# Optimization experiments

Hardware: AMD Instinct MI355X
Metric: run time of the kernel (lower is better)

The kernel has to match this reference:

```python
import jax, jax.numpy as jnp
import numpy as np

N_QUBITS = 12
N_LAYERS = 3
FEAT_DIM = 64
BATCH = 8192
PI = float(np.pi)


def setup_inputs() -> dict:
    key = jax.random.key(0)
    k1, k2, k3 = jax.random.split(key, 3)
    x = jax.random.normal(k1, (BATCH, FEAT_DIM), dtype=jnp.float32)
    # nn.Linear(feature_dim, num_qubits, bias=False) weight: [num_qubits, feature_dim]
    W = jax.random.normal(k2, (N_QUBITS, FEAT_DIM), dtype=jnp.float32) * (1.0 / np.sqrt(FEAT_DIM))
    # quantum params ~ Uniform(-pi, pi), shape [num_layers, num_qubits, 2] (RY, RZ angles)
    quantum_params = jax.random.uniform(k3, (N_LAYERS, N_QUBITS, 2), minval=-PI, maxval=PI, dtype=jnp.float32)
    return {"x": x, "W": W, "quantum_params": quantum_params}


def _halves(st, ax):
    a0 = jax.lax.index_in_dim(st, 0, ax, keepdims=True)
    a1 = jax.lax.index_in_dim(st, 1, ax, keepdims=True)
    return a0, a1


def _ry(st, theta, q, n):
    # RY(t) = [[cos t/2, -sin t/2], [sin t/2, cos t/2]] on qubit q (wire 0 = most significant)
    ax = q + 1
    c = jnp.cos(theta * 0.5)
    s = jnp.sin(theta * 0.5)
    if jnp.ndim(c) > 0:  # per-batch angles -> broadcast [B,1,...,1]
        c = c.reshape(c.shape + (1,) * n)
        s = s.reshape(s.shape + (1,) * n)
    a0, a1 = _halves(st, ax)
    return jnp.concatenate([c * a0 - s * a1, s * a0 + c * a1], axis=ax)


def _rz(st, theta, q, n):
    # RZ(t) = diag(e^{-i t/2}, e^{i t/2}) on qubit q
    ax = q + 1
    ph = jnp.exp(-0.5j * theta)
    a0, a1 = _halves(st, ax)
    return jnp.concatenate([ph * a0, jnp.conj(ph) * a1], axis=ax)


def _cnot(st, ctrl, tgt):
    # flip target amplitudes on the control=1 subspace
    ax_c, ax_t = ctrl + 1, tgt + 1
    s0, s1 = _halves(st, ax_c)
    return jnp.concatenate([s0, jnp.flip(s1, axis=ax_t)], axis=ax_c)


def reference(x, W, quantum_params):
    n = N_QUBITS
    # feature projection + tanh squashing to [-pi, pi]
    angles = jnp.tanh(x @ W.T) * PI  # [B, n]
    B = x.shape[0]
    # batched state vector |0...0>, shape [B] + [2]*n (wire 0 most significant, PennyLane convention)
    st = jnp.zeros((B,) + (2,) * n, dtype=jnp.complex64)
    st = st.at[(slice(None),) + (0,) * n].set(1.0)
    for layer in range(N_LAYERS):
        # data (re)uploading: RY(features[i]) each layer since data_reuploading=True
        for q in range(n):
            st = _ry(st, angles[:, q], q, n)
        # variational rotations
        for q in range(n):
            st = _ry(st, quantum_params[layer, q, 0], q, n)
            st = _rz(st, quantum_params[layer, q, 1], q, n)
        # ring entanglement
        for q in range(n):
            st = _cnot(st, q, (q + 1) % n)
    probs = jnp.real(st * jnp.conj(st))  # [B] + [2]*n
    outs = []
    for q in range(n):  # <PauliZ_q> = p(bit_q=0) - p(bit_q=1)
        axes = tuple(a for a in range(1, n + 1) if a != q + 1)
        p = probs.sum(axis=axes)  # [B, 2]
        outs.append(p[:, 0] - p[:, 1])
    return jnp.stack(outs, axis=1).astype(x.dtype)  # [B, n]
```

## Files before the change

kernel.cpp:

```cpp
#include <hip/hip_runtime.h>

namespace {

constexpr int NQ = 12;
constexpr int NL = 3;
constexpr int FEAT = 64;
constexpr float PI_F = 3.14159265358979323846f;

typedef float f2 __attribute__((ext_vector_type(2)));

constexpr int par12(unsigned x) { int p = 0; for (int i = 0; i < 12; ++i) p ^= (int)((x >> i) & 1u); return p; }
constexpr int lead12(unsigned x) { for (int k = 11; k >= 0; --k) if ((x >> k) & 1u) return k; return -1; }

struct Ech { unsigned v[16] = {}; int n = 0; };
constexpr unsigned ech_reduce(const Ech& E, unsigned x) {
  for (int i = 0; i < E.n; ++i) { int lb = lead12(E.v[i]); if (lb >= 0 && ((x >> lb) & 1u)) x ^= E.v[i]; }
  return x;
}
constexpr bool ech_add(Ech& E, unsigned x) {
  unsigned r = ech_reduce(E, x);
  if (!r) return false;
  int lb = lead12(r);
  int pos = E.n;
  for (int i = 0; i < E.n; ++i) { if (lead12(E.v[i]) < lb) { pos = i; break; } }
  for (int i = E.n; i > pos; --i) E.v[i] = E.v[i - 1];
  E.v[pos] = r; E.n++;
  return true;
}

constexpr unsigned apmat(const unsigned* rows, unsigned v) {
  unsigned o = 0; for (int k = 0; k < 12; ++k) if (par12(rows[k] & v)) o |= 1u << k; return o;
}
constexpr bool inv12(const unsigned* in, unsigned* out) {
  unsigned a[12] = {}, b[12] = {};
  for (int k = 0; k < 12; ++k) { a[k] = in[k]; b[k] = 1u << k; }
  for (int c = 0; c < 12; ++c) {
    int p = -1;
    for (int r = c; r < 12; ++r) if ((a[r] >> c) & 1u) { p = r; break; }
    if (p < 0) return false;
    unsigned t = a[c]; a[c] = a[p]; a[p] = t; t = b[c]; b[c] = b[p]; b[p] = t;
    for (int r = 0; r < 12; ++r) if (r != c && ((a[r] >> c) & 1u)) { a[r] ^= a[c]; b[r] ^= b[c]; }
  }
  for (int k = 0; k < 12; ++k) out[k] = b[k];
  return true;
}
constexpr unsigned dropb(unsigned x, int t) {
  unsigned lm = (1u << t) - 1u;
  return (x & lm) | ((x >> 1) & (0x7FFu & ~lm));
}

struct Logical {
  unsigned m[NL][NQ] = {}, rv[NL][NQ] = {}, rf[NQ] = {};
  bool ok = false;
};
constexpr Logical compute_raw() {
  Logical mp{};
  unsigned col[NQ] = {}, row[NQ] = {};
  for (int b = 0; b < NQ; ++b) { col[b] = 1u << b; row[b] = 1u << b; }
  mp.ok = true;
  for (int L = 0; L < NL; ++L) {
    for (int q = 0; q < NQ; ++q) {
      mp.m[L][q]  = col[NQ - 1 - q];
      mp.rv[L][q] = row[NQ - 1 - q];
      if (par12(mp.m[L][q] & mp.rv[L][q]) != 1) mp.ok = false;
    }
    for (int q = 0; q < NQ; ++q) {
      int bc = NQ - 1 - q;
      int bt = NQ - 1 - ((q + 1) % NQ);
      col[bc] ^= col[bt];
      row[bt] ^= row[bc];
    }
  }
  for (int q = 0; q < NQ; ++q) mp.rf[q] = row[NQ - 1 - q];
  return mp;
}

struct Plan {
  unsigned l0m[NQ] = {}, l0r[NQ] = {};
  unsigned gm[4][6] = {};
  unsigned gr[4][6] = {};
  unsigned rf[NQ] = {};
  unsigned phi[4][6] = {};
  unsigned coffE[4][64] = {};
  int cb[4] = {};
  bool ok = false;
};

constexpr bool findH(const Ech& G, unsigned rho, unsigned& out) {
  for (unsigned t = 0; t < 12; ++t) {
    unsigned v = 1u << t;
    if (par12(v & rho) == 0 && ech_reduce(G, v)) { out = v; return true; }
  }
  for (unsigned v = 1; v < 4096u; ++v) {
    if (par12(v & rho) == 0 && ech_reduce(G, v)) { out = v; return true; }
  }
  return false;
}

constexpr Plan build_plan() {
  Logical raw = compute_raw();
  Plan P{};
  P.ok = raw.ok;
  for (int q = 0; q < NQ; ++q) { P.l0m[q] = raw.m[0][q]; P.l0r[q] = raw.rv[0][q]; }
  unsigned fwd[12] = {}, invc[12] = {};
  for (int k = 0; k < 12; ++k) { fwd[k] = 1u << k; invc[k] = 1u << k; }
  for (int ph = 0; ph < 4; ++ph) {
    const int L = 1 + ph / 2, q0 = (ph % 2) * 6;
    unsigned ml[6] = {};
    for (int i = 0; i < 6; ++i) ml[i] = raw.m[L][q0 + i];
    bool done = false;
    for (int cbi = 5; cbi >= 0 && !done; --cbi) {
      unsigned rho = fwd[6 + cbi];
      bool bad = false;
      int idx = -1;
      for (int i = 0; i < 6; ++i) if (par12(ml[i] & rho)) { idx = i; break; }
      unsigned uc = 0;
      Ech W{};
      if (idx >= 0) {
        uc = ml[idx];
        for (int i = 0; i < 6; ++i) {
          if (i == idx) continue;
          unsigned w = par12(ml[i] & rho) ? (ml[i] ^ uc) : ml[i];
          ech_add(W, w);
        }
        if (W.n > 5) bad = true;
      } else {
        for (int i = 0; i < 6; ++i) ech_add(W, ml[i]);
        if (W.n > 5) bad = true;
        if (!bad) {
          bool got = false;
          for (unsigned t = 0; t < 12 && !got; ++t) {
            unsigned v = 1u << t;
            if (par12(v & rho)) { uc = v; got = true; }
          }
          if (!got) bad = true;
        }
      }
      if (bad) continue;
      Ech G{};
      for (int i = 0; i < W.n && !bad; ++i) if (!ech_add(G, W.v[i])) bad = true;
      if (!bad && !ech_add(G, uc)) bad = true;
      if (bad) continue;
      unsigned regH[5] = {};
      int nH = W.n;
      for (int i = 0; i < nH; ++i) regH[i] = W.v[i];
      for (int slot = nH; slot < 5 && !bad; ++slot) {
        unsigned v = 0;
        if (!findH(G, rho, v)) { bad = true; break; }
        regH[slot] = v; ech_add(G, v);
      }
      if (bad) continue;
      unsigned lam[6] = {};
      for (int j = 0; j < 6 && !bad; ++j) {
        unsigned cand = invc[j];
        if (par12(cand & rho) != 0 || !ech_reduce(G, cand)) {
          if (!findH(G, rho, cand)) { bad = true; break; }
        }
        lam[j] = cand; ech_add(G, cand);
      }
      if (bad) continue;
      unsigned ncols[12] = {};
      for (int j = 0; j < 6; ++j) ncols[j] = lam[j];
      {
        int w = 0;
        for (int k = 0; k < 6; ++k) ncols[6 + k] = (k == cbi) ? uc : regH[w++];
      }
      unsigned Mrows[12] = {};
      for (int k = 0; k < 12; ++k) {
        unsigned r = 0;
        for (int j = 0; j < 12; ++j) r |= ((ncols[j] >> k) & 1u) << j;
        Mrows[k] = r;
      }
      unsigned fnew[12] = {};
      if (!inv12(Mrows, fnew)) continue;
      bool okp = true;
      unsigned gmv[6] = {}, grv[6] = {};
      for (int i = 0; i < 6 && okp; ++i) {
        unsigned SM = apmat(fnew, ml[i]);
        if (SM & 63u) okp = false;
        unsigned sg = 0;
        for (int k = 0; k < 12; ++k) if (par12(raw.rv[L][q0 + i] & ncols[k])) sg |= 1u << k;
        if (par12(SM & sg) != 1) okp = false;
        gmv[i] = SM; grv[i] = sg;
      }
      unsigned phj[6] = {}, Ust[6] = {};
      for (int j = 0; j < 6 && okp; ++j) {
        phj[j] = apmat(fwd, lam[j]);
        if ((phj[j] >> (6 + cbi)) & 1u) okp = false;
      }
      for (int k = 0; k < 6 && okp; ++k) {
        Ust[k] = apmat(fwd, ncols[6 + k]);
        if (((Ust[k] >> (6 + cbi)) & 1u) != (unsigned)(k == cbi ? 1 : 0)) okp = false;
      }
      if (!okp) continue;
      P.cb[ph] = cbi;
      for (int j = 0; j < 6; ++j) P.phi[ph][j] = phj[j];
      for (int rp = 0; rp < 64; ++rp) {
        unsigned psi = 0;
        for (int i = 0; i < 6; ++i) if ((rp >> i) & 1) psi ^= Ust[i];
        P.coffE[ph][rp] = dropb(psi, 6 + cbi);
      }
      for (int i = 0; i < 6; ++i) { P.gm[ph][i] = gmv[i]; P.gr[ph][i] = grv[i]; }
      for (int k = 0; k < 12; ++k) { fwd[k] = fnew[k]; invc[k] = ncols[k]; }
      done = true;
    }
    if (!done) { P.ok = false; return P; }
  }
  for (int q = 0; q < NQ; ++q) {
    unsigned sg = 0;
    for (int k = 0; k < 12; ++k) if (par12(raw.rf[q] & invc[k])) sg |= 1u << k;
    P.rf[q] = sg;
  }
  return P;
}

constexpr Plan PLAN = build_plan();
static_assert(PLAN.ok, "plan construction failed");

__device__ __forceinline__ f2 pk_mul_bl(f2 a, f2 u) {
  f2 d;
  asm("v_pk_mul_f32 %0, %1, %2 op_sel:[0,0] op_sel_hi:[1,0]" : "=v"(d) : "v"(a), "v"(u));
  return d;
}
__device__ __forceinline__ f2 pk_fma_rot_p(f2 a, f2 u, f2 c) {
  f2 d;
  asm("v_pk_fma_f32 %0, %1, %2, %3 op_sel:[1,1,0] op_sel_hi:[0,1,1] neg_lo:[1,0,0]"
      : "=v"(d) : "v"(a), "v"(u), "v"(c));
  return d;
}
__device__ __forceinline__ f2 pk_fma_rot_m(f2 a, f2 u, f2 c) {
  f2 d;
  asm("v_pk_fma_f32 %0, %1, %2, %3 op_sel:[1,1,0] op_sel_hi:[0,1,1] neg_hi:[1,0,0]"
      : "=v"(d) : "v"(a), "v"(u), "v"(c));
  return d;
}
__device__ __forceinline__ f2 pk_fma_bl_p(f2 p, f2 v, f2 c) {
  f2 d;
  asm("v_pk_fma_f32 %0, %1, %2, %3 op_sel:[0,0,0] op_sel_hi:[1,0,1]"
      : "=v"(d) : "v"(p), "v"(v), "v"(c));
  return d;
}
__device__ __forceinline__ f2 pk_fma_bl_m(f2 p, f2 v, f2 c) {
  f2 d;
  asm("v_pk_fma_f32 %0, %1, %2, %3 op_sel:[0,0,0] op_sel_hi:[1,0,1] neg_lo:[0,1,0] neg_hi:[0,1,0]"
      : "=v"(d) : "v"(p), "v"(v), "v"(c));
  return d;
}
__device__ __forceinline__ f2 pk_mul_d(f2 a, f2 b) {
  f2 d;
  asm("v_pk_mul_f32 %0, %1, %2" : "=v"(d) : "v"(a), "v"(b));
  return d;
}
__device__ __forceinline__ f2 pk_fma_d(f2 a, f2 b, f2 c) {
  f2 d;
  asm("v_pk_fma_f32 %0, %1, %2, %3" : "=v"(d) : "v"(a), "v"(b), "v"(c));
  return d;
}

template<bool REAL>
__device__ __forceinline__ f2 updp(f2 a, f2 p, f2 u, f2 v) {
  if constexpr (REAL) return pk_fma_bl_p(p, v, pk_mul_bl(a, u));
  else return pk_fma_rot_p(p, v, pk_fma_bl_p(p, v, pk_fma_rot_p(a, u, pk_mul_bl(a, u))));
}
template<bool REAL>
__device__ __forceinline__ f2 updm(f2 a, f2 p, f2 u, f2 v) {
  if constexpr (REAL) return pk_fma_bl_m(p, v, pk_mul_bl(a, u));
  else return pk_fma_rot_p(p, v, pk_fma_bl_m(p, v, pk_fma_rot_m(a, u, pk_mul_bl(a, u))));
}

template<unsigned MLO>
__device__ __forceinline__ float shx(float v, int lane4) {
  if constexpr (MLO == 0u) {
    return v;
  } else if constexpr (MLO < 32u) {
    constexpr int off = (int)((MLO << 10) | 0x1fu);
    return __int_as_float(__builtin_amdgcn_ds_swizzle(__float_as_int(v), off));
  } else {
    int addr = lane4 ^ (int)(MLO << 2);
    return __int_as_float(__builtin_amdgcn_ds_bpermute(addr, __float_as_int(v)));
  }
}

template<unsigned M, unsigned R, int NREG, bool REAL>
__device__ __forceinline__ void gate(f2* st, float ghalf, float phihalf, int lane, int lane4) {
  float s, c;
  __sincosf(ghalf, &s, &c);
  constexpr unsigned MHI = (M >> 6) & 63u;
  constexpr unsigned MLO = M & 63u;
  constexpr unsigned RHI = (R >> 6) & 63u;
  constexpr unsigned RLO = R & 63u;
  float sL = (__popc((int)(RLO & (unsigned)lane)) & 1) ? -1.f : 1.f;
  f2 u, v;
  if constexpr (REAL) {
    u.x = c;       u.y = 0.f;
    v.x = -s * sL; v.y = 0.f;
  } else {
    float sf, cf;
    __sincosf(phihalf, &sf, &cf);
    u.x = c * cf;         u.y = (-c * sf) * sL;
    v.x = (-s * cf) * sL; v.y = s * sf;
  }
  if constexpr (MLO == 0u) {
    constexpr unsigned TB = MHI & (~MHI + 1u);
    #pragma unroll
    for (int r = 0; r < NREG; ++r) {
      if ((r & (int)TB) == 0) {
        int r2 = r ^ (int)MHI;
        const bool rp = ((__builtin_popcount((unsigned)r & RHI)) & 1) != 0;
        f2 a = st[r], b = st[r2];
        st[r]  = rp ? updm<REAL>(a, b, u, v) : updp<REAL>(a, b, u, v);
        st[r2] = rp ? updp<REAL>(b, a, u, v) : updm<REAL>(b, a, u, v);
      }
    }
  } else {
    #pragma unroll
    for (int r = 0; r < NREG; ++r) {
      f2 p;
      p.x = shx<MLO>(st[r].x, lane4);
      p.y = shx<MLO>(st[r].y, lane4);
      const bool rp = ((__builtin_popcount((unsigned)r & RHI)) & 1) != 0;
      st[r] = rp ? updm<REAL>(st[r], p, u, v) : updp<REAL>(st[r], p, u, v);
    }
  }
}

template<int Q>
__device__ __forceinline__ void l0_lane(f2* st, const float* ang, const float* __restrict__ qp, int lane, int lane4) {
  if constexpr (Q < NQ) {
    constexpr unsigned M = PLAN.l0m[Q];
    if constexpr (M < 64u) {
      gate<M, PLAN.l0r[Q], 1, false>(st, 0.5f * (ang[Q] + qp[Q * 2 + 0]), 0.5f * qp[Q * 2 + 1], lane, lane4);
    }
    l0_lane<Q + 1>(st, ang, qp, lane, lane4);
  }
}
template<int Q, unsigned DONE>
__device__ __forceinline__ void l0_reg(f2* st, const float* ang, const float* __restrict__ qp) {
  if constexpr (Q < NQ) {
    constexpr unsigned M = PLAN.l0m[Q];
    if constexpr (M >= 64u) {
      constexpr unsigned TB = (M >> 6) & 63u;
      float sh = 0.5f * (ang[Q] + qp[Q * 2 + 0]);
      float ph = 0.5f * qp[Q * 2 + 1];
      float s, c, sf, cf;
      __sincosf(sh, &s, &c);
      __sincosf(ph, &sf, &cf);
      f2 u0; u0.x = c * cf; u0.y = -c * sf;
      f2 u1; u1.x = s * cf; u1.y =  s * sf;
      #pragma unroll
      for (int r = 0; r < 64; ++r) {
        if ((r & ~(int)DONE & 63) == 0) {
          f2 a = st[r];
          int r2 = r | (int)TB;
          st[r]  = pk_fma_rot_p(a, u0, pk_mul_bl(a, u0));
          st[r2] = pk_fma_rot_p(a, u1, pk_mul_bl(a, u1));
        }
      }
      l0_reg<Q + 1, DONE | TB>(st, ang, qp);
    } else {
      l0_reg<Q + 1, DONE>(st, ang, qp);
    }
  }
}

__device__ __forceinline__ int pad(int a) { return a + (a >> 5); }

template<int PH>
__device__ __forceinline__ void remap(f2* st, f2* lds, int lane) {
  constexpr int b = PLAN.cb[PH];
  constexpr unsigned LM6 = (1u << b) - 1u;
  constexpr unsigned LM = (1u << (6 + b)) - 1u;
  unsigned B = 0;
  #pragma unroll
  for (int j = 0; j < 6; ++j) B ^= (unsigned)(-(int)((lane >> j) & 1)) & PLAN.phi[PH][j];
  unsigned rBe = (B & LM) | ((B >> 1) & (0x7FFu & ~LM));
  #pragma unroll
  for (int s = 0; s < 2; ++s) {
    #pragma unroll
    for (int r = 0; r < 64; ++r) {
      if (((r >> b) & 1) == s) {
        const int cr = (r & (int)LM6) | ((r >> 1) & (31 & ~(int)LM6));
        lds[pad((cr << 6) | lane)] = st[r];
      }
    }
    asm volatile("s_waitcnt lgkmcnt(0)" ::: "memory");
    #pragma unroll
    for (int rp = 0; rp < 64; ++rp) {
      if (((rp >> b) & 1) == s) {
        st[rp] = lds[pad((int)(rBe ^ PLAN.coffE[PH][rp]))];
      }
    }
    asm volatile("s_waitcnt lgkmcnt(0)" ::: "memory");
  }
}

template<int PH, int I>
__device__ __forceinline__ void do_phase(f2* st, const float* ang, const float* __restrict__ qp, int lane, int lane4) {
  if constexpr (I < 6) {
    constexpr int L = 1 + PH / 2;
    constexpr bool REAL = (L == NL - 1);
    constexpr int q = (PH % 2) * 6 + I;
    constexpr unsigned M = PLAN.gm[PH][I];
    constexpr unsigned R = PLAN.gr[PH][I];
    float th0 = qp[(L * NQ + q) * 2 + 0];
    float ph1 = REAL ? 0.f : 0.5f * qp[(L * NQ + q) * 2 + 1];
    gate<M, R, 64, REAL>(st, 0.5f * (ang[q] + th0), ph1, lane, lane4);
    do_phase<PH, I + 1>(st, ang, qp, lane, lane4);
  }
}

__device__ __forceinline__ float redsum(float v, int lane4) {
  v += shx<1>(v, lane4);
  v += shx<2>(v, lane4);
  v += shx<4>(v, lane4);
  v += shx<8>(v, lane4);
  v += shx<16>(v, lane4);
  v += shx<32>(v, lane4);
  return v;
}
__device__ __forceinline__ float fast_tanh(float x) {
  float e = __expf(2.f * x);
  float r = __builtin_amdgcn_rcpf(e + 1.f);
  return 1.f - 2.f * r;
}

template<int Q>
__device__ __forceinline__ void finish(const f2* acc6, float& outv, int lane, int lane4) {
  if constexpr (Q < NQ) {
    constexpr unsigned RLO = PLAN.rf[Q] & 63u;
    float a = (Q & 1) ? acc6[Q / 2].y : acc6[Q / 2].x;
    float sLn = (__popc((int)(RLO & (unsigned)lane)) & 1) ? -a : a;
    float t = redsum(sLn, lane4);
    if (lane == Q) outv = t;
    finish<Q + 1>(acc6, outv, lane, lane4);
  }
}

__global__ __launch_bounds__(64, 1) void qtr_kernel(const float* __restrict__ x,
                                                    const float* __restrict__ W,
                                                    const float* __restrict__ qp,
                                                    float* __restrict__ out) {
  __shared__ f2 ldsb[2112];
  int b = blockIdx.x;
  int lane = threadIdx.x;
  int lane4 = lane << 2;

  float xv = x[b * FEAT + lane];
  float ang[NQ];
  #pragma unroll
  for (int q = 0; q < NQ; ++q) {
    float prod = redsum(xv * W[q * FEAT + lane], lane4);
    ang[q] = PI_F * fast_tanh(prod);
  }

  f2 st[64];
  st[0].x = (lane == 0) ? 1.f : 0.f;
  st[0].y = 0.f;

  l0_lane<0>(st, ang, qp, lane, lane4);
  l0_reg<0, 0u>(st, ang, qp);

  remap<0>(st, ldsb, lane);
  do_phase<0, 0>(st, ang, qp, lane, lane4);
  remap<1>(st, ldsb, lane);
  do_phase<1, 0>(st, ang, qp, lane, lane4);
  remap<2>(st, ldsb, lane);
  do_phase<2, 0>(st, ang, qp, lane, lane4);
  remap<3>(st, ldsb, lane);
  do_phase<3, 0>(st, ang, qp, lane, lane4);

  f2 acc6[6];
  #pragma unroll
  for (int j = 0; j < 6; ++j) { acc6[j].x = 0.f; acc6[j].y = 0.f; }
  #pragma unroll
  for (int r = 0; r < 64; ++r) {
    f2 q2 = pk_mul_d(st[r], st[r]);
    float p = q2.x + q2.y;
    f2 pp; pp.x = p; pp.y = p;
    #pragma unroll
    for (int j = 0; j < 6; ++j) {
      const bool n0 = ((__builtin_popcount(((PLAN.rf[2 * j]     >> 6) & 63u) & (unsigned)r)) & 1) != 0;
      const bool n1 = ((__builtin_popcount(((PLAN.rf[2 * j + 1] >> 6) & 63u) & (unsigned)r)) & 1) != 0;
      f2 sg; sg.x = n0 ? -1.f : 1.f; sg.y = n1 ? -1.f : 1.f;
      acc6[j] = pk_fma_d(pp, sg, acc6[j]);
    }
  }

  float outv = 0.f;
  finish<0>(acc6, outv, lane, lane4);

  if (lane < NQ) out[b * NQ + lane] = outv;
}

}

extern "C" void kernel_launch(void* const* d_in, const int* in_sizes, int n_in,
                              void* d_out, int out_size, void* d_ws, size_t ws_size,
                              hipStream_t stream) {
  const float* x  = (const float*)d_in[0];
  const float* W  = (const float*)d_in[1];
  const float* qp = (const float*)d_in[2];
  float* out = (float*)d_out;
  qtr_kernel<<<8192, 64, 0, stream>>>(x, W, qp, out);
}
```

Before: 131.9 us.

## Split each sample's state vector across two waves with LDS exchange

Each block now uses two 64-lane waves, and each wave holds half of the 4096-amplitude state (32 registers instead of 64). Gates on the top register bit become cross-wave exchanges through LDS with __syncthreads, and remaps and the final reduction are rewritten for the split layout. The aim is to halve register pressure per wave and double parallelism per sample. The cost is extra block-level barriers, LDS traffic for cross-wave gates, and duplicated angle computation in both waves.

```diff
diff --git a/kernel.cpp b/kernel.cpp
--- a/kernel.cpp
+++ b/kernel.cpp
@@ -217,6 +217,10 @@
 constexpr Plan PLAN = build_plan();
 static_assert(PLAN.ok, "plan construction failed");
 
+constexpr int find_qw() { for (int q = 0; q < NQ; ++q) if (((PLAN.l0m[q] >> 6) & 63u) == 32u) return q; return -1; }
+constexpr int QW = find_qw();
+static_assert(QW >= 0, "no wave-bit l0 gate found");
+
 __device__ __forceinline__ f2 pk_mul_bl(f2 a, f2 u) {
   f2 d;
   asm("v_pk_mul_f32 %0, %1, %2 op_sel:[0,0] op_sel_hi:[1,0]" : "=v"(d) : "v"(a), "v"(u));
@@ -267,6 +271,7 @@
   if constexpr (REAL) return pk_fma_bl_m(p, v, pk_mul_bl(a, u));
   else return pk_fma_rot_p(p, v, pk_fma_bl_m(p, v, pk_fma_rot_m(a, u, pk_mul_bl(a, u))));
 }
+__device__ __forceinline__ f2 cmul(f2 a, f2 u) { return pk_fma_rot_p(a, u, pk_mul_bl(a, u)); }
 
 template<unsigned MLO>
 __device__ __forceinline__ float shx(float v, int lane4) {
@@ -281,16 +286,34 @@
   }
 }
 
-template<unsigned M, unsigned R, int NREG, bool REAL>
-__device__ __forceinline__ void gate(f2* st, float ghalf, float phihalf, int lane, int lane4) {
+template<unsigned M, unsigned R, bool REAL>
+__device__ __forceinline__ void gate1(f2* st, float ghalf, float phihalf, int lane, int lane4) {
   float s, c;
   __sincosf(ghalf, &s, &c);
-  constexpr unsigned MHI = (M >> 6) & 63u;
   constexpr unsigned MLO = M & 63u;
-  constexpr unsigned RHI = (R >> 6) & 63u;
   constexpr unsigned RLO = R & 63u;
   float sL = (__popc((int)(RLO & (unsigned)lane)) & 1) ? -1.f : 1.f;
   f2 u, v;
+  float sf, cf;
+  __sincosf(phihalf, &sf, &cf);
+  u.x = c * cf;         u.y = (-c * sf) * sL;
+  v.x = (-s * cf) * sL; v.y = s * sf;
+  f2 p;
+  p.x = shx<MLO>(st[0].x, lane4);
+  p.y = shx<MLO>(st[0].y, lane4);
+  st[0] = updp<REAL>(st[0], p, u, v);
+}
+
+template<unsigned R, bool REAL>
+__device__ __forceinline__ void make_uv(float ghalf, float phihalf, int l6, int w, f2& u, f2& v) {
+  constexpr unsigned RHI = (R >> 6) & 63u;
+  constexpr unsigned RLO = R & 63u;
+  constexpr unsigned S5 = (RHI >> 5) & 1u;
+  float s, c;
+  __sincosf(ghalf, &s, &c);
+  int par = __popc((int)(RLO & (unsigned)l6));
+  if constexpr (S5 != 0u) par ^= w;
+  float sL = (par & 1) ? -1.f : 1.f;
   if constexpr (REAL) {
     u.x = c;       u.y = 0.f;
     v.x = -s * sL; v.y = 0.f;
@@ -300,27 +323,72 @@
     u.x = c * cf;         u.y = (-c * sf) * sL;
     v.x = (-s * cf) * sL; v.y = s * sf;
   }
-  if constexpr (MLO == 0u) {
-    constexpr unsigned TB = MHI & (~MHI + 1u);
-    #pragma unroll
-    for (int r = 0; r < NREG; ++r) {
-      if ((r & (int)TB) == 0) {
-        int r2 = r ^ (int)MHI;
-        const bool rp = ((__builtin_popcount((unsigned)r & RHI)) & 1) != 0;
-        f2 a = st[r], b = st[r2];
-        st[r]  = rp ? updm<REAL>(a, b, u, v) : updp<REAL>(a, b, u, v);
-        st[r2] = rp ? updp<REAL>(b, a, u, v) : updm<REAL>(b, a, u, v);
-      }
-    }
-  } else {
-    #pragma unroll
-    for (int r = 0; r < NREG; ++r) {
-      f2 p;
-      p.x = shx<MLO>(st[r].x, lane4);
-      p.y = shx<MLO>(st[r].y, lane4);
-      const bool rp = ((__builtin_popcount((unsigned)r & RHI)) & 1) != 0;
-      st[r] = rp ? updm<REAL>(st[r], p, u, v) : updp<REAL>(st[r], p, u, v);
-    }
+}
+
+template<unsigned M, unsigned R, bool REAL>
+__device__ __forceinline__ void gate32_local(f2* st, float ghalf, float phihalf, int l6, int w) {
+  constexpr unsigned MHI = (M >> 6) & 31u;
+  constexpr unsigned RHI5 = (R >> 6) & 31u;
+  static_assert(MHI != 0u, "empty local mask");
+  f2 u, v;
+  make_uv<R, REAL>(ghalf, phihalf, l6, w, u, v);
+  constexpr unsigned TB = MHI & (~MHI + 1u);
+  #pragma unroll
+  for (int rl = 0; rl < 32; ++rl) {
+    if ((rl & (int)TB) == 0) {
+      int rl2 = rl ^ (int)MHI;
+      const bool rp = ((__builtin_popcount((unsigned)rl & RHI5)) & 1) != 0;
+      f2 a = st[rl], b = st[rl2];
+      st[rl]  = rp ? updm<REAL>(a, b, u, v) : updp<REAL>(a, b, u, v);
+      st[rl2] = rp ? updp<REAL>(b, a, u, v) : updm<REAL>(b, a, u, v);
+    }
+  }
+}
+
+template<unsigned M, unsigned R, bool REAL>
+__device__ __forceinline__ void gate32_cross(f2* st, f2* lds, float ghalf, float phihalf, int l6, int w) {
+  constexpr unsigned MHI = (M >> 6) & 63u;
+  constexpr unsigned ML5 = MHI & 31u;
+  constexpr unsigned RHI5 = (R >> 6) & 31u;
+  constexpr int FLIP = (int)((ML5 >> 4) & 1u);
+  f2 u, v;
+  make_uv<R, REAL>(ghalf, phihalf, l6, w, u, v);
+  #pragma unroll
+  for (int t = 0; t < 2; ++t) {
+    if (w == 0) {
+      #pragma unroll
+      for (int rr = 0; rr < 16; ++rr) {
+        const int rlm = (t << 4) | rr;
+        lds[(rr << 6) | l6] = st[rlm];
+      }
+    } else {
+      #pragma unroll
+      for (int rr = 0; rr < 16; ++rr) {
+        const int rlm = ((t ^ FLIP) << 4) | rr;
+        const int i = (rlm ^ (int)ML5) & 15;
+        lds[1024 | (i << 6) | l6] = st[rlm];
+      }
+    }
+    __syncthreads();
+    if (w == 0) {
+      #pragma unroll
+      for (int rr = 0; rr < 16; ++rr) {
+        const int rlm = (t << 4) | rr;
+        f2 p = lds[1024 | (rr << 6) | l6];
+        const bool rp = ((__builtin_popcount((unsigned)rlm & RHI5)) & 1) != 0;
+        st[rlm] = rp ? updm<REAL>(st[rlm], p, u, v) : updp<REAL>(st[rlm], p, u, v);
+      }
+    } else {
+      #pragma unroll
+      for (int rr = 0; rr < 16; ++rr) {
+        const int rlm = ((t ^ FLIP) << 4) | rr;
+        const int i = (rlm ^ (int)ML5) & 15;
+        f2 p = lds[(i << 6) | l6];
+        const bool rp = ((__builtin_popcount((unsigned)rlm & RHI5)) & 1) != 0;
+        st[rlm] = rp ? updm<REAL>(st[rlm], p, u, v) : updp<REAL>(st[rlm], p, u, v);
+      }
+    }
+    __syncthreads();
   }
 }
 
@@ -329,17 +397,17 @@
   if constexpr (Q < NQ) {
     constexpr unsigned M = PLAN.l0m[Q];
     if constexpr (M < 64u) {
-      gate<M, PLAN.l0r[Q], 1, false>(st, 0.5f * (ang[Q] + qp[Q * 2 + 0]), 0.5f * qp[Q * 2 + 1], lane, lane4);
+      gate1<M, PLAN.l0r[Q], false>(st, 0.5f * (ang[Q] + qp[Q * 2 + 0]), 0.5f * qp[Q * 2 + 1], lane, lane4);
     }
     l0_lane<Q + 1>(st, ang, qp, lane, lane4);
   }
 }
 template<int Q, unsigned DONE>
-__device__ __forceinline__ void l0_reg(f2* st, const float* ang, const float* __restrict__ qp) {
+__device__ __forceinline__ void l0_reg32(f2* st, const float* ang, const float* __restrict__ qp) {
   if constexpr (Q < NQ) {
     constexpr unsigned M = PLAN.l0m[Q];
-    if constexpr (M >= 64u) {
-      constexpr unsigned TB = (M >> 6) & 63u;
+    if constexpr (M >= 64u && ((M >> 6) & 63u) != 32u) {
+      constexpr unsigned TB = (M >> 6) & 31u;
       float sh = 0.5f * (ang[Q] + qp[Q * 2 + 0]);
       float ph = 0.5f * qp[Q * 2 + 1];
       float s, c, sf, cf;
@@ -348,17 +416,17 @@
       f2 u0; u0.x = c * cf; u0.y = -c * sf;
       f2 u1; u1.x = s * cf; u1.y =  s * sf;
       #pragma unroll
-      for (int r = 0; r < 64; ++r) {
-        if ((r & ~(int)DONE & 63) == 0) {
+      for (int r = 0; r < 32; ++r) {
+        if ((r & ~(int)DONE & 31) == 0) {
           f2 a = st[r];
           int r2 = r | (int)TB;
-          st[r]  = pk_fma_rot_p(a, u0, pk_mul_bl(a, u0));
-          st[r2] = pk_fma_rot_p(a, u1, pk_mul_bl(a, u1));
-        }
-      }
-      l0_reg<Q + 1, DONE | TB>(st, ang, qp);
+          st[r]  = cmul(a, u0);
+          st[r2] = cmul(a, u1);
+        }
+      }
+      l0_reg32<Q + 1, DONE | TB>(st, ang, qp);
     } else {
-      l0_reg<Q + 1, DONE>(st, ang, qp);
+      l0_reg32<Q + 1, DONE>(st, ang, qp);
     }
   }
 }
@@ -366,46 +434,82 @@
 __device__ __forceinline__ int pad(int a) { return a + (a >> 5); }
 
 template<int PH>
-__device__ __forceinline__ void remap(f2* st, f2* lds, int lane) {
+__device__ __forceinline__ void remap32(f2* st, f2* lds, int l6, int w) {
   constexpr int b = PLAN.cb[PH];
-  constexpr unsigned LM6 = (1u << b) - 1u;
   constexpr unsigned LM = (1u << (6 + b)) - 1u;
   unsigned B = 0;
   #pragma unroll
-  for (int j = 0; j < 6; ++j) B ^= (unsigned)(-(int)((lane >> j) & 1)) & PLAN.phi[PH][j];
+  for (int j = 0; j < 6; ++j) B ^= (unsigned)(-(int)((l6 >> j) & 1)) & PLAN.phi[PH][j];
   unsigned rBe = (B & LM) | ((B >> 1) & (0x7FFu & ~LM));
-  #pragma unroll
-  for (int s = 0; s < 2; ++s) {
+  if constexpr (b == 5) {
     #pragma unroll
-    for (int r = 0; r < 64; ++r) {
-      if (((r >> b) & 1) == s) {
-        const int cr = (r & (int)LM6) | ((r >> 1) & (31 & ~(int)LM6));
-        lds[pad((cr << 6) | lane)] = st[r];
-      }
-    }
-    asm volatile("s_waitcnt lgkmcnt(0)" ::: "memory");
+    for (int s = 0; s < 2; ++s) {
+      if (w == s) {
+        #pragma unroll
+        for (int rl = 0; rl < 32; ++rl) lds[pad((rl << 6) | l6)] = st[rl];
+      }
+      __syncthreads();
+      if (w == s) {
+        #pragma unroll
+        for (int rl = 0; rl < 32; ++rl) st[rl] = lds[pad((int)(rBe ^ PLAN.coffE[PH][rl | (s << 5)]))];
+      }
+      __syncthreads();
+    }
+  } else {
+    constexpr unsigned LM5 = (1u << b) - 1u;
     #pragma unroll
-    for (int rp = 0; rp < 64; ++rp) {
-      if (((rp >> b) & 1) == s) {
-        st[rp] = lds[pad((int)(rBe ^ PLAN.coffE[PH][rp]))];
-      }
-    }
-    asm volatile("s_waitcnt lgkmcnt(0)" ::: "memory");
+    for (int s = 0; s < 2; ++s) {
+      if (w == 0) {
+        #pragma unroll
+        for (int rl = 0; rl < 32; ++rl) {
+          if (((rl >> b) & 1) == s) {
+            const int cr = (rl & (int)LM5) | ((rl >> 1) & (15 & ~(int)LM5));
+            lds[pad((cr << 6) | l6)] = st[rl];
+          }
+        }
+      } else {
+        #pragma unroll
+        for (int rl = 0; rl < 32; ++rl) {
+          if (((rl >> b) & 1) == s) {
+            const int cr = 16 | (rl & (int)LM5) | ((rl >> 1) & (15 & ~(int)LM5));
+            lds[pad((cr << 6) | l6)] = st[rl];
+          }
+        }
+      }
+      __syncthreads();
+      if (w == 0) {
+        #pragma unroll
+        for (int rl = 0; rl < 32; ++rl) {
+          if (((rl >> b) & 1) == s) st[rl] = lds[pad((int)(rBe ^ PLAN.coffE[PH][rl]))];
+        }
+      } else {
+        #pragma unroll
+        for (int rl = 0; rl < 32; ++rl) {
+          if (((rl >> b) & 1) == s) st[rl] = lds[pad((int)(rBe ^ PLAN.coffE[PH][rl | 32]))];
+        }
+      }
+      __syncthreads();
+    }
   }
 }
 
 template<int PH, int I>
-__device__ __forceinline__ void do_phase(f2* st, const float* ang, const float* __restrict__ qp, int lane, int lane4) {
+__device__ __forceinline__ void do_phase(f2* st, f2* lds, const float* ang, const float* __restrict__ qp, int l6, int w) {
   if constexpr (I < 6) {
     constexpr int L = 1 + PH / 2;
     constexpr bool REAL = (L == NL - 1);
     constexpr int q = (PH % 2) * 6 + I;
     constexpr unsigned M = PLAN.gm[PH][I];
     constexpr unsigned R = PLAN.gr[PH][I];
+    static_assert((M & 63u) == 0u, "phase gate not reg-local");
     float th0 = qp[(L * NQ + q) * 2 + 0];
     float ph1 = REAL ? 0.f : 0.5f * qp[(L * NQ + q) * 2 + 1];
-    gate<M, R, 64, REAL>(st, 0.5f * (ang[q] + th0), ph1, lane, lane4);
-    do_phase<PH, I + 1>(st, ang, qp, lane, lane4);
+    float g = 0.5f * (ang[q] + th0);
+    if constexpr (((M >> 11) & 1u) != 0u)
+      gate32_cross<M, R, REAL>(st, lds, g, ph1, l6, w);
+    else
+      gate32_local<M, R, REAL>(st, g, ph1, l6, w);
+    do_phase<PH, I + 1>(st, lds, ang, qp, l6, w);
   }
 }
 
@@ -425,71 +529,102 @@
 }
 
 template<int Q>
-__device__ __forceinline__ void finish(const f2* acc6, float& outv, int lane, int lane4) {
+__device__ __forceinline__ void finish(const f2* acc6, float& outv, int l6, int lane4, int w) {
   if constexpr (Q < NQ) {
     constexpr unsigned RLO = PLAN.rf[Q] & 63u;
+    constexpr unsigned S11 = (PLAN.rf[Q] >> 11) & 1u;
     float a = (Q & 1) ? acc6[Q / 2].y : acc6[Q / 2].x;
-    float sLn = (__popc((int)(RLO & (unsigned)lane)) & 1) ? -a : a;
+    int par = __popc((int)(RLO & (unsigned)l6));
+    if constexpr (S11 != 0u) par ^= w;
+    float sLn = (par & 1) ? -a : a;
     float t = redsum(sLn, lane4);
-    if (lane == Q) outv = t;
-    finish<Q + 1>(acc6, outv, lane, lane4);
-  }
-}
-
-__global__ __launch_bounds__(64, 1) void qtr_kernel(const float* __restrict__ x,
-                                                    const float* __restrict__ W,
-                                                    const float* __restrict__ qp,
-                                                    float* __restrict__ out) {
+    if (l6 == Q) outv = t;
+    finish<Q + 1>(acc6, outv, l6, lane4, w);
+  }
+}
+
+__global__ __launch_bounds__(128) void qtr_kernel(const float* __restrict__ x,
+                                                  const float* __restrict__ W,
+                                                  const float* __restrict__ qp,
+                                                  float* __restrict__ out) {
   __shared__ f2 ldsb[2112];
-  int b = blockIdx.x;
-  int lane = threadIdx.x;
-  int lane4 = lane << 2;
-
-  float xv = x[b * FEAT + lane];
+  int bb = blockIdx.x;
+  int tid = threadIdx.x;
+  int w = tid >> 6;
+  int l6 = tid & 63;
+  int lane4 = l6 << 2;
+
+  float xv = x[bb * FEAT + l6];
   float ang[NQ];
   #pragma unroll
   for (int q = 0; q < NQ; ++q) {
-    float prod = redsum(xv * W[q * FEAT + lane], lane4);
+    float prod = redsum(xv * W[q * FEAT + l6], lane4);
     ang[q] = PI_F * fast_tanh(prod);
   }
 
-  f2 st[64];
-  st[0].x = (lane == 0) ? 1.f : 0.f;
-  st[0].y = 0.f;
-
-  l0_lane<0>(st, ang, qp, lane, lane4);
-  l0_reg<0, 0u>(st, ang, qp);
-
-  remap<0>(st, ldsb, lane);
-  do_phase<0, 0>(st, ang, qp, lane, lane4);
-  remap<1>(st, ldsb, lane);
-  do_phase<1, 0>(st, ang, qp, lane, lane4);
-  remap<2>(st, ldsb, lane);
-  do_phase<2, 0>(st, ang, qp, lane, lane4);
-  remap<3>(st, ldsb, lane);
-  do_phase<3, 0>(st, ang, qp, lane, lane4);
+  f2 st[32];
+  if (w == 0) {
+    st[0].x = (l6 == 0) ? 1.f : 0.f;
+    st[0].y = 0.f;
+    l0_lane<0>(st, ang, qp, l6, lane4);
+    l0_reg32<0, 0u>(st, ang, qp);
+  }
+  {
+    float sh = 0.5f * (ang[QW] + qp[QW * 2 + 0]);
+    float ph = 0.5f * qp[QW * 2 + 1];
+    float s, c, sf, cf;
+    __sincosf(sh, &s, &c);
+    __sincosf(ph, &sf, &cf);
+    f2 u0; u0.x = c * cf; u0.y = -c * sf;
+    f2 u1; u1.x = s * cf; u1.y =  s * sf;
+    if (w == 0) {
+      #pragma unroll
+      for (int rl = 0; rl < 32; ++rl) ldsb[(rl << 6) | l6] = st[rl];
+    }
+    __syncthreads();
+    if (w == 0) {
+      #pragma unroll
+      for (int rl = 0; rl < 32; ++rl) st[rl] = cmul(st[rl], u0);
+    } else {
+      #pragma unroll
+      for (int rl = 0; rl < 32; ++rl) st[rl] = cmul(ldsb[(rl << 6) | l6], u1);
+    }
+    __syncthreads();
+  }
+
+  remap32<0>(st, ldsb, l6, w);
+  do_phase<0, 0>(st, ldsb, ang, qp, l6, w);
+  remap32<1>(st, ldsb, l6, w);
+  do_phase<1, 0>(st, ldsb, ang, qp, l6, w);
+  remap32<2>(st, ldsb, l6, w);
+  do_phase<2, 0>(st, ldsb, ang, qp, l6, w);
+  remap32<3>(st, ldsb, l6, w);
+  do_phase<3, 0>(st, ldsb, ang, qp, l6, w);
 
   f2 acc6[6];
   #pragma unroll
   for (int j = 0; j < 6; ++j) { acc6[j].x = 0.f; acc6[j].y = 0.f; }
   #pragma unroll
-  for (int r = 0; r < 64; ++r) {
-    f2 q2 = pk_mul_d(st[r], st[r]);
+  for (int rl = 0; rl < 32; ++rl) {
+    f2 q2 = pk_mul_d(st[rl], st[rl]);
     float p = q2.x + q2.y;
     f2 pp; pp.x = p; pp.y = p;
     #pragma unroll
     for (int j = 0; j < 6; ++j) {
-      const bool n0 = ((__builtin_popcount(((PLAN.rf[2 * j]     >> 6) & 63u) & (unsigned)r)) & 1) != 0;
-      const bool n1 = ((__builtin_popcount(((PLAN.rf[2 * j + 1] >> 6) & 63u) & (unsigned)r)) & 1) != 0;
+      const bool n0 = ((__builtin_popcount(((PLAN.rf[2 * j]     >> 6) & 31u) & (unsigned)rl)) & 1) != 0;
+      const bool n1 = ((__builtin_popcount(((PLAN.rf[2 * j + 1] >> 6) & 31u) & (unsigned)rl)) & 1) != 0;
       f2 sg; sg.x = n0 ? -1.f : 1.f; sg.y = n1 ? -1.f : 1.f;
       acc6[j] = pk_fma_d(pp, sg, acc6[j]);
     }
   }
 
   float outv = 0.f;
-  finish<0>(acc6, outv, lane, lane4);
-
-  if (lane < NQ) out[b * NQ + lane] = outv;
+  finish<0>(acc6, outv, l6, lane4, w);
+
+  float* fl = (float*)ldsb;
+  if (l6 < NQ) fl[w * 16 + l6] = outv;
+  __syncthreads();
+  if (tid < NQ) out[bb * NQ + tid] = fl[tid] + fl[16 + tid];
 }
 
 }
@@ -501,5 +636,5 @@
   const float* W  = (const float*)d_in[1];
   const float* qp = (const float*)d_in[2];
   float* out = (float*)d_out;
-  qtr_kernel<<<8192, 64, 0, stream>>>(x, W, qp, out);
-}
+  qtr_kernel<<<8192, 128, 0, stream>>>(x, W, qp, out);
+}
```

New measurement: 178.6 us. 1.35x slower.
